# Kernel tuning notes

Measured on AMD Instinct MI355X. Metric: run time of the kernel, lower is better.

The kernel has to match this reference:

```python
import jax, jax.numpy as jnp
import numpy as np

N, E, F_IN, H, C = 50000, 800000, 128, 64, 10

def setup_inputs() -> dict:
    key = jax.random.key(0)
    ks = jax.random.split(key, 8)
    x = jax.random.normal(ks[0], (N, F_IN), dtype=jnp.float32)
    edge_index = jax.random.randint(ks[1], (2, E), 0, N, dtype=jnp.int32)
    edge_weight = jax.random.uniform(ks[2], (E,), dtype=jnp.float32)
    W1 = jax.random.normal(ks[3], (H, F_IN), dtype=jnp.float32) * 0.05
    W2 = jax.random.normal(ks[4], (H, H), dtype=jnp.float32) * 0.05
    W3 = jax.random.normal(ks[5], (C, H), dtype=jnp.float32) * 0.05
    b1 = jnp.zeros((H,), jnp.float32)
    b2 = jnp.zeros((H,), jnp.float32)
    b3 = jnp.zeros((C,), jnp.float32)
    return {"x": x, "edge_index": edge_index, "edge_weight": edge_weight,
            "W1": W1, "b1": b1, "W2": W2, "b2": b2, "W3": W3, "b3": b3}

def reference(x, edge_index, edge_weight, W1, b1, W2, b2, W3, b3):
    n = x.shape[0]
    row, col = edge_index[0], edge_index[1]
    # GCN symmetric normalization (add_self_loops=False): deg from edge weights on col
    deg = jax.ops.segment_sum(edge_weight, col, num_segments=n)  # [N]
    dinv = jnp.where(deg > 0, jax.lax.rsqrt(deg), 0.0)
    norm = dinv[row] * edge_weight * dinv[col]  # [E]

    def gcn_layer(h, W, b):
        h = h @ W.T                               # linear transform [N, out]
        msg = h[row] * norm[:, None]              # gather + scale   [E, out]
        agg = jax.ops.segment_sum(msg, col, num_segments=n)  # scatter-add [N, out]
        return agg + b

    h = gcn_layer(x, W1, b1)
    h = gcn_layer(h, W2, b2)
    logits = gcn_layer(h, W3, b3)
    soft = jax.nn.softmax(logits, axis=1)
    return logits, soft
```

## Files before the change

kernel.cpp:

```cpp
#include <hip/hip_runtime.h>
#include <hip/hip_fp16.h>

#define N_NODES 50000
#define N_EDGES 800000
#define F_IN    128
#define H_DIM   64
#define C_DIM   10
#define CPAD    16
#define CAP     48
#define BLOCK   256
#define BIN_NODES 256
#define NBINS   196
#define STRIDE  4480
#define E_BLK   2048
#define ABLOCKS ((N_EDGES + E_BLK - 1) / E_BLK)
#define DGB     (N_NODES / 16)
#define WB      ((N_NODES * 64) / 256)
#define POISON  ((int)0xAAAAAAAA)

__device__ __forceinline__ int unbase(int v) {
    return ((unsigned)v < 65536u) ? v : v - POISON;
}

__device__ __forceinline__ int   prow(unsigned v) { return (int)(v >> 16); }
__device__ __forceinline__ float pw(unsigned v)   {
    return __half2float(__ushort_as_half((unsigned short)(v & 0xFFFFu)));
}

__global__ __launch_bounds__(256) void k_binA(const int* __restrict__ rows,
                                              const int* __restrict__ cols,
                                              const float* __restrict__ ew,
                                              const float* __restrict__ W1,
                                              const float* __restrict__ b1,
                                              const float* __restrict__ W2,
                                              const float* __restrict__ b2,
                                              const float* __restrict__ W3,
                                              int* __restrict__ bucketCnt,
                                              unsigned* __restrict__ regionA,
                                              unsigned short* __restrict__ regionC,
                                              float* __restrict__ T2g,
                                              float* __restrict__ v1g,
                                              float* __restrict__ v2g) {
    const int tid = threadIdx.x;
    if (blockIdx.x < ABLOCKS) {
        __shared__ unsigned       sA[E_BLK];
        __shared__ unsigned short sC[E_BLK];
        __shared__ int hcnt[NBINS];
        __shared__ int lbase[NBINS];
        __shared__ int gb[NBINS];
        for (int i = tid; i < NBINS; i += BLOCK) hcnt[i] = 0;
        __syncthreads();

        const int e0 = blockIdx.x * E_BLK;
        unsigned rw[8];
        unsigned cl[8];
#pragma unroll
        for (int j = 0; j < 8; ++j) {
            int e = e0 + j * BLOCK + tid;
            if (e < N_EDGES) {
                int   c = cols[e];
                int   r = rows[e];
                float w = ew[e];
                rw[j] = ((unsigned)r << 16) | (unsigned)__half_as_ushort(__float2half(w));
                int lr = atomicAdd(&hcnt[c >> 8], 1);
                cl[j] = (unsigned)c | ((unsigned)lr << 16);
            } else {
                cl[j] = 0xFFFFFFFFu;
            }
        }
        __syncthreads();

        if (tid < 64) {
            int run = 0;
            for (int base = 0; base < NBINS; base += 64) {
                int i = base + tid;
                int v = (i < NBINS) ? hcnt[i] : 0;
                int s = v;
#pragma unroll
                for (int off = 1; off < 64; off <<= 1) {
                    int t = __shfl_up(s, off);
                    if (tid >= off) s += t;
                }
                if (i < NBINS) lbase[i] = run + s - v;
                run += __shfl(s, 63);
            }
        }
        __syncthreads();

#pragma unroll
        for (int j = 0; j < 8; ++j) {
            if (cl[j] != 0xFFFFFFFFu) {
                int c  = (int)(cl[j] & 0xFFFFu);
                int lr = (int)(cl[j] >> 16);
                int pos = lbase[c >> 8] + lr;
                sA[pos] = rw[j];
                sC[pos] = (unsigned short)c;
            }
        }
        if (tid < NBINS) gb[tid] = unbase(atomicAdd(&bucketCnt[tid], hcnt[tid]));
        __syncthreads();

        const int total = lbase[NBINS - 1] + hcnt[NBINS - 1];
        for (int i = tid; i < total; i += BLOCK) {
            int c = sC[i];
            int b = c >> 8;
            int gpos = gb[b] + (i - lbase[b]);
            if (gpos < STRIDE) {
                size_t p = (size_t)b * STRIDE + gpos;
                regionA[p] = sA[i];
                regionC[p] = (unsigned short)c;
            }
        }
        return;
    }

    __shared__ float u[C_DIM * H_DIM];
    for (int idx = tid; idx < C_DIM * H_DIM; idx += BLOCK) {
        int c = idx >> 6, j = idx & 63;
        float a = 0.f;
#pragma unroll
        for (int k = 0; k < H_DIM; ++k) a += W3[c * H_DIM + k] * W2[k * H_DIM + j];
        u[idx] = a;
    }
    __syncthreads();
    for (int idx = tid; idx < C_DIM * F_IN; idx += BLOCK) {
        int c = idx >> 7, f = idx & 127;
        float a = 0.f;
#pragma unroll
        for (int k = 0; k < H_DIM; ++k) a += u[c * H_DIM + k] * W1[k * F_IN + f];
        T2g[idx] = a;
    }
    if (tid < C_DIM) {
        float a = 0.f, b = 0.f;
#pragma unroll
        for (int k = 0; k < H_DIM; ++k) {
            a += u[tid * H_DIM + k] * b1[k];
            b += W3[tid * H_DIM + k] * b2[k];
        }
        v1g[tid] = a;
        v2g[tid] = b;
    }
}

__global__ __launch_bounds__(256) void k_binB(const int* __restrict__ bucketCnt,
                                              const unsigned* __restrict__ regionA,
                                              const unsigned short* __restrict__ regionC,
                                              float2* __restrict__ meta,
                                              unsigned* __restrict__ edata) {
    __shared__ unsigned sdata[BIN_NODES * CAP];
    __shared__ int   lcnt[BIN_NODES];
    __shared__ float wsum[BIN_NODES];
    const int tid = threadIdx.x;
    const int b   = blockIdx.x;
    if (tid < BIN_NODES) { lcnt[tid] = 0; wsum[tid] = 0.f; }
    __syncthreads();

    int tot = unbase(bucketCnt[b]);
    if (tot > STRIDE) tot = STRIDE;
    const size_t segBase = (size_t)b * STRIDE;
    for (int i = tid; i < tot; i += BLOCK) {
        unsigned e = regionA[segBase + i];
        int nl = (int)regionC[segBase + i] - b * BIN_NODES;
        int r = atomicAdd(&lcnt[nl], 1);
        if (r < CAP) sdata[nl * CAP + r] = e;
        atomicAdd(&wsum[nl], pw(e));
    }
    __syncthreads();

    const int n0 = b * BIN_NODES;
    const int nvalid = min(N_NODES - n0, BIN_NODES);
    if (tid < nvalid) {
        int c0 = min(lcnt[tid], CAP);
        int cp = (c0 + 15) & ~15;
        if (cp > CAP) cp = CAP;
        for (int r = c0; r < cp; ++r) sdata[tid * CAP + r] = 0u;
        float d = wsum[tid];
        meta[n0 + tid] = make_float2(d > 0.f ? rsqrtf(d) : 0.f, (float)cp);
    }
    __syncthreads();

    int4* dst = reinterpret_cast<int4*>(edata + (size_t)n0 * CAP);
    const int4* src = reinterpret_cast<const int4*>(sdata);
    const int nvec = nvalid * CAP / 4;
    for (int i = tid; i < nvec; i += BLOCK) dst[i] = src[i];
}

__global__ __launch_bounds__(256) void k_dg(const float* __restrict__ x,
                                            const float* __restrict__ T2g,
                                            const float2* __restrict__ meta,
                                            __half* __restrict__ bufA) {
    __shared__ float ts[16 * 132];
    __shared__ float xs[16][132];
    const int tid = threadIdx.x;
    const int n0 = blockIdx.x * 16;

    for (int i = tid; i < 16 * F_IN; i += BLOCK) {
        int c = i >> 7;
        ts[c * 132 + (i & 127)] = (c < C_DIM) ? T2g[i] : 0.f;
    }
    for (int i = tid; i < 16 * 32; i += BLOCK) {
        int ln = i >> 5, f4 = i & 31;
        float4 v = reinterpret_cast<const float4*>(x)[(n0 + ln) * 32 + f4];
        *reinterpret_cast<float4*>(&xs[ln][f4 * 4]) = v;
    }
    __syncthreads();

    const int g = tid >> 4;
    const int c = tid & 15;
    const int n = n0 + g;
    const float di = meta[n].x;

    const float4* tsv = reinterpret_cast<const float4*>(&ts[c * 132]);
    const float4* xv  = reinterpret_cast<const float4*>(&xs[g][0]);
    float a = 0.f;
#pragma unroll 8
    for (int f4 = 0; f4 < 32; ++f4) {
        float4 xx = xv[f4], tt = tsv[f4];
        a += xx.x * tt.x + xx.y * tt.y + xx.z * tt.z + xx.w * tt.w;
    }
    float outv = (c < C_DIM) ? a * di : (c == 10 ? di : 0.f);
    bufA[n * CPAD + c] = __float2half(outv);
}

__global__ __launch_bounds__(256) void k_gather(const float2* __restrict__ meta,
                                                const unsigned* __restrict__ edata,
                                                const __half* __restrict__ zin,
                                                __half* __restrict__ zout) {
    int n = (blockIdx.x * 256 + threadIdx.x) >> 6;
    if (n >= N_NODES) return;
    int lane = threadIdx.x & 63;
    int sub = lane >> 4, c = lane & 15;
    float2 m = meta[n];
    float di = m.x;
    int iters = ((int)m.y) >> 4;
    int base = n * CAP + sub;
    float acc = 0.f;
#pragma unroll
    for (int i = 0; i < 3; ++i) {
        if (i < iters) {
            int k = base + i * 16;
            unsigned e0 = edata[k];
            unsigned e1 = edata[k + 4];
            unsigned e2 = edata[k + 8];
            unsigned e3 = edata[k + 12];
            acc += pw(e0) * __half2float(zin[prow(e0) * CPAD + c]);
            acc += pw(e1) * __half2float(zin[prow(e1) * CPAD + c]);
            acc += pw(e2) * __half2float(zin[prow(e2) * CPAD + c]);
            acc += pw(e3) * __half2float(zin[prow(e3) * CPAD + c]);
        }
    }
    acc += __shfl_xor(acc, 32);
    acc += __shfl_xor(acc, 16);
    if (lane < 16) zout[n * CPAD + lane] = __float2half(acc * di * di);
}

__global__ __launch_bounds__(256) void k_final(const float2* __restrict__ meta,
                                               const unsigned* __restrict__ edata,
                                               const __half* __restrict__ zin,
                                               const __half* __restrict__ s1buf,
                                               const float* __restrict__ v1,
                                               const float* __restrict__ v2,
                                               const float* __restrict__ b3,
                                               float* __restrict__ logits,
                                               float* __restrict__ soft) {
    int n = (blockIdx.x * 256 + threadIdx.x) >> 6;
    if (n >= N_NODES) return;
    int lane = threadIdx.x & 63;
    int sub = lane >> 4, c = lane & 15;
    float2 m = meta[n];
    float di = m.x;
    int iters = ((int)m.y) >> 4;
    int base = n * CAP + sub;
    float acc = 0.f;
#pragma unroll
    for (int i = 0; i < 3; ++i) {
        if (i < iters) {
            int k = base + i * 16;
            unsigned e0 = edata[k];
            unsigned e1 = edata[k + 4];
            unsigned e2 = edata[k + 8];
            unsigned e3 = edata[k + 12];
            acc += pw(e0) * __half2float(zin[prow(e0) * CPAD + c]);
            acc += pw(e1) * __half2float(zin[prow(e1) * CPAD + c]);
            acc += pw(e2) * __half2float(zin[prow(e2) * CPAD + c]);
            acc += pw(e3) * __half2float(zin[prow(e3) * CPAD + c]);
        }
    }
    acc += __shfl_xor(acc, 32);
    acc += __shfl_xor(acc, 16);

    float r  = di > 0.f ? 1.0f / di : 0.f;
    float a1 = __half2float(s1buf[n * CPAD + 10]) * r;
    float a2 = __half2float(zin[n * CPAD + 10]) * r;
    float l = (c < C_DIM) ? di * acc + a2 * v1[c] + a1 * v2[c] + b3[c] : -1e30f;
    float mx = l;
#pragma unroll
    for (int d = 8; d >= 1; d >>= 1) mx = fmaxf(mx, __shfl_xor(mx, d));
    float ev = (c < C_DIM) ? __expf(l - mx) : 0.f;
    float s = ev;
#pragma unroll
    for (int d = 8; d >= 1; d >>= 1) s += __shfl_xor(s, d);
    if (lane < C_DIM) {
        logits[n * C_DIM + lane] = l;
        soft[n * C_DIM + lane]   = ev / s;
    }
}

extern "C" void kernel_launch(void* const* d_in, const int* in_sizes, int n_in,
                              void* d_out, int out_size, void* d_ws, size_t ws_size,
                              hipStream_t stream) {
    const float* x  = (const float*)d_in[0];
    const int*   ei = (const int*)d_in[1];
    const float* ew = (const float*)d_in[2];
    const float* W1 = (const float*)d_in[3];
    const float* b1 = (const float*)d_in[4];
    const float* W2 = (const float*)d_in[5];
    const float* b2 = (const float*)d_in[6];
    const float* W3 = (const float*)d_in[7];
    const float* b3 = (const float*)d_in[8];
    const int* rows = ei;
    const int* cols = ei + N_EDGES;

    char* ws = (char*)d_ws;
    size_t off = 0;
    auto alloc = [&](size_t bytes) { void* q = ws + off; off += (bytes + 15) & ~size_t(15); return q; };

    float2*         meta      = (float2*)         alloc((size_t)N_NODES * 8);
    __half*         bufA      = (__half*)         alloc((size_t)N_NODES * CPAD * 2);
    __half*         bufB      = (__half*)         alloc((size_t)N_NODES * CPAD * 2);
    float*          T2g       = (float*)          alloc(C_DIM * F_IN * 4);
    float*          v1        = (float*)          alloc(64);
    float*          v2        = (float*)          alloc(64);
    int*            bucketCnt = (int*)            alloc(NBINS * 4);
    unsigned*       regionA   = (unsigned*)       alloc((size_t)NBINS * STRIDE * 4);
    unsigned short* regionC   = (unsigned short*) alloc((size_t)NBINS * STRIDE * 2);
    unsigned*       edata     = (unsigned*)       alloc((size_t)N_NODES * CAP * 4);

    float* logits = (float*)d_out;
    float* soft   = logits + N_NODES * C_DIM;

    k_binA<<<ABLOCKS + 1, 256, 0, stream>>>(rows, cols, ew, W1, b1, W2, b2, W3,
                                            bucketCnt, regionA, regionC, T2g, v1, v2);
    k_binB<<<NBINS, 256, 0, stream>>>(bucketCnt, regionA, regionC, meta, edata);
    k_dg<<<DGB, 256, 0, stream>>>(x, T2g, meta, bufA);
    k_gather<<<WB, 256, 0, stream>>>(meta, edata, bufA, bufB);
    k_gather<<<WB, 256, 0, stream>>>(meta, edata, bufB, bufA);
    k_final<<<WB, 256, 0, stream>>>(meta, edata, bufA, bufB, v1, v2, b3,
                                    logits, soft);
}
```

Baseline: 166.7 us.

## Fuse projection, gather passes and softmax into one cooperative persistent kernel

Replaces the four separate launches (k_dg, two k_gather, k_final) with a single cooperative kernel that runs each stage in grid-stride loops and separates the stages with grid.sync(). This removes three kernel launch boundaries and their tail effects. It also halves the bin size used for edge bucketing (128 nodes per bin, more bins, smaller stride), which changes the binning stage's parallelism and shared-memory footprint. In exchange, grid-wide barriers cost something, and a persistent grid sized from occupancy may underuse the GPU compared with oversubscribed launches.

```diff
diff --git a/kernel.cpp b/kernel.cpp
--- a/kernel.cpp
+++ b/kernel.cpp
@@ -1,5 +1,8 @@
 #include <hip/hip_runtime.h>
 #include <hip/hip_fp16.h>
+#include <hip/hip_cooperative_groups.h>
+
+namespace cg = cooperative_groups;
 
 #define N_NODES 50000
 #define N_EDGES 800000
@@ -9,13 +12,12 @@
 #define CPAD    16
 #define CAP     48
 #define BLOCK   256
-#define BIN_NODES 256
-#define NBINS   196
-#define STRIDE  4480
+#define BIN_NODES 128
+#define NBINS   ((N_NODES + BIN_NODES - 1) / BIN_NODES)
+#define STRIDE  2560
 #define E_BLK   2048
 #define ABLOCKS ((N_EDGES + E_BLK - 1) / E_BLK)
 #define DGB     (N_NODES / 16)
-#define WB      ((N_NODES * 64) / 256)
 #define POISON  ((int)0xAAAAAAAA)
 
 __device__ __forceinline__ int unbase(int v) {
@@ -62,7 +64,7 @@
                 int   r = rows[e];
                 float w = ew[e];
                 rw[j] = ((unsigned)r << 16) | (unsigned)__half_as_ushort(__float2half(w));
-                int lr = atomicAdd(&hcnt[c >> 8], 1);
+                int lr = atomicAdd(&hcnt[c >> 7], 1);
                 cl[j] = (unsigned)c | ((unsigned)lr << 16);
             } else {
                 cl[j] = 0xFFFFFFFFu;
@@ -92,18 +94,19 @@
             if (cl[j] != 0xFFFFFFFFu) {
                 int c  = (int)(cl[j] & 0xFFFFu);
                 int lr = (int)(cl[j] >> 16);
-                int pos = lbase[c >> 8] + lr;
+                int pos = lbase[c >> 7] + lr;
                 sA[pos] = rw[j];
                 sC[pos] = (unsigned short)c;
             }
         }
-        if (tid < NBINS) gb[tid] = unbase(atomicAdd(&bucketCnt[tid], hcnt[tid]));
+        for (int i = tid; i < NBINS; i += BLOCK)
+            gb[i] = unbase(atomicAdd(&bucketCnt[i], hcnt[i]));
         __syncthreads();
 
         const int total = lbase[NBINS - 1] + hcnt[NBINS - 1];
         for (int i = tid; i < total; i += BLOCK) {
             int c = sC[i];
-            int b = c >> 8;
+            int b = c >> 7;
             int gpos = gb[b] + (i - lbase[b]);
             if (gpos < STRIDE) {
                 size_t p = (size_t)b * STRIDE + gpos;
@@ -185,124 +188,132 @@
     for (int i = tid; i < nvec; i += BLOCK) dst[i] = src[i];
 }
 
-__global__ __launch_bounds__(256) void k_dg(const float* __restrict__ x,
-                                            const float* __restrict__ T2g,
+__device__ __forceinline__ void gather_pass(int wid, int nW, int lane,
                                             const float2* __restrict__ meta,
-                                            __half* __restrict__ bufA) {
+                                            const unsigned* __restrict__ edata,
+                                            const __half* __restrict__ zin,
+                                            __half* __restrict__ zout) {
+    const int sub = lane >> 4, c = lane & 15;
+    for (int n = wid; n < N_NODES; n += nW) {
+        float2 m = meta[n];
+        int iters = ((int)m.y) >> 4;
+        int base = n * CAP + sub;
+        float acc = 0.f;
+#pragma unroll
+        for (int i = 0; i < 3; ++i) {
+            if (i < iters) {
+                int k = base + i * 16;
+                unsigned e0 = edata[k];
+                unsigned e1 = edata[k + 4];
+                unsigned e2 = edata[k + 8];
+                unsigned e3 = edata[k + 12];
+                acc += pw(e0) * __half2float(zin[prow(e0) * CPAD + c]);
+                acc += pw(e1) * __half2float(zin[prow(e1) * CPAD + c]);
+                acc += pw(e2) * __half2float(zin[prow(e2) * CPAD + c]);
+                acc += pw(e3) * __half2float(zin[prow(e3) * CPAD + c]);
+            }
+        }
+        acc += __shfl_xor(acc, 32);
+        acc += __shfl_xor(acc, 16);
+        if (lane < 16) zout[n * CPAD + lane] = __float2half(acc * m.x * m.x);
+    }
+}
+
+__global__ __launch_bounds__(256) void k_main(const float* __restrict__ x,
+                                              const float* __restrict__ T2g,
+                                              const float2* __restrict__ meta,
+                                              const unsigned* __restrict__ edata,
+                                              __half* __restrict__ bufA,
+                                              __half* __restrict__ bufB,
+                                              const float* __restrict__ v1,
+                                              const float* __restrict__ v2,
+                                              const float* __restrict__ b3,
+                                              float* __restrict__ logits,
+                                              float* __restrict__ soft) {
+    cg::grid_group grid = cg::this_grid();
+    const int tid  = threadIdx.x;
+    const int lane = tid & 63;
+    const int wid  = blockIdx.x * 4 + (tid >> 6);
+    const int nW   = gridDim.x * 4;
+
     __shared__ float ts[16 * 132];
     __shared__ float xs[16][132];
-    const int tid = threadIdx.x;
-    const int n0 = blockIdx.x * 16;
-
     for (int i = tid; i < 16 * F_IN; i += BLOCK) {
         int c = i >> 7;
         ts[c * 132 + (i & 127)] = (c < C_DIM) ? T2g[i] : 0.f;
     }
-    for (int i = tid; i < 16 * 32; i += BLOCK) {
-        int ln = i >> 5, f4 = i & 31;
-        float4 v = reinterpret_cast<const float4*>(x)[(n0 + ln) * 32 + f4];
-        *reinterpret_cast<float4*>(&xs[ln][f4 * 4]) = v;
-    }
-    __syncthreads();
-
-    const int g = tid >> 4;
-    const int c = tid & 15;
-    const int n = n0 + g;
-    const float di = meta[n].x;
-
-    const float4* tsv = reinterpret_cast<const float4*>(&ts[c * 132]);
-    const float4* xv  = reinterpret_cast<const float4*>(&xs[g][0]);
-    float a = 0.f;
+    const int g = tid >> 4, c = tid & 15;
+    for (int t = blockIdx.x; t < DGB; t += gridDim.x) {
+        __syncthreads();
+        const int n0 = t * 16;
+        for (int i = tid; i < 16 * 32; i += BLOCK) {
+            int ln = i >> 5, f4 = i & 31;
+            float4 v = reinterpret_cast<const float4*>(x)[(n0 + ln) * 32 + f4];
+            *reinterpret_cast<float4*>(&xs[ln][f4 * 4]) = v;
+        }
+        __syncthreads();
+        const int n = n0 + g;
+        const float di = meta[n].x;
+        const float4* tsv = reinterpret_cast<const float4*>(&ts[c * 132]);
+        const float4* xv  = reinterpret_cast<const float4*>(&xs[g][0]);
+        float a = 0.f;
 #pragma unroll 8
-    for (int f4 = 0; f4 < 32; ++f4) {
-        float4 xx = xv[f4], tt = tsv[f4];
-        a += xx.x * tt.x + xx.y * tt.y + xx.z * tt.z + xx.w * tt.w;
-    }
-    float outv = (c < C_DIM) ? a * di : (c == 10 ? di : 0.f);
-    bufA[n * CPAD + c] = __float2half(outv);
-}
-
-__global__ __launch_bounds__(256) void k_gather(const float2* __restrict__ meta,
-                                                const unsigned* __restrict__ edata,
-                                                const __half* __restrict__ zin,
-                                                __half* __restrict__ zout) {
-    int n = (blockIdx.x * 256 + threadIdx.x) >> 6;
-    if (n >= N_NODES) return;
-    int lane = threadIdx.x & 63;
-    int sub = lane >> 4, c = lane & 15;
-    float2 m = meta[n];
-    float di = m.x;
-    int iters = ((int)m.y) >> 4;
-    int base = n * CAP + sub;
-    float acc = 0.f;
-#pragma unroll
-    for (int i = 0; i < 3; ++i) {
-        if (i < iters) {
-            int k = base + i * 16;
-            unsigned e0 = edata[k];
-            unsigned e1 = edata[k + 4];
-            unsigned e2 = edata[k + 8];
-            unsigned e3 = edata[k + 12];
-            acc += pw(e0) * __half2float(zin[prow(e0) * CPAD + c]);
-            acc += pw(e1) * __half2float(zin[prow(e1) * CPAD + c]);
-            acc += pw(e2) * __half2float(zin[prow(e2) * CPAD + c]);
-            acc += pw(e3) * __half2float(zin[prow(e3) * CPAD + c]);
-        }
-    }
-    acc += __shfl_xor(acc, 32);
-    acc += __shfl_xor(acc, 16);
-    if (lane < 16) zout[n * CPAD + lane] = __float2half(acc * di * di);
-}
-
-__global__ __launch_bounds__(256) void k_final(const float2* __restrict__ meta,
-                                               const unsigned* __restrict__ edata,
-                                               const __half* __restrict__ zin,
-                                               const __half* __restrict__ s1buf,
-                                               const float* __restrict__ v1,
-                                               const float* __restrict__ v2,
-                                               const float* __restrict__ b3,
-                                               float* __restrict__ logits,
-                                               float* __restrict__ soft) {
-    int n = (blockIdx.x * 256 + threadIdx.x) >> 6;
-    if (n >= N_NODES) return;
-    int lane = threadIdx.x & 63;
-    int sub = lane >> 4, c = lane & 15;
-    float2 m = meta[n];
-    float di = m.x;
-    int iters = ((int)m.y) >> 4;
-    int base = n * CAP + sub;
-    float acc = 0.f;
-#pragma unroll
-    for (int i = 0; i < 3; ++i) {
-        if (i < iters) {
-            int k = base + i * 16;
-            unsigned e0 = edata[k];
-            unsigned e1 = edata[k + 4];
-            unsigned e2 = edata[k + 8];
-            unsigned e3 = edata[k + 12];
-            acc += pw(e0) * __half2float(zin[prow(e0) * CPAD + c]);
-            acc += pw(e1) * __half2float(zin[prow(e1) * CPAD + c]);
-            acc += pw(e2) * __half2float(zin[prow(e2) * CPAD + c]);
-            acc += pw(e3) * __half2float(zin[prow(e3) * CPAD + c]);
-        }
-    }
-    acc += __shfl_xor(acc, 32);
-    acc += __shfl_xor(acc, 16);
-
-    float r  = di > 0.f ? 1.0f / di : 0.f;
-    float a1 = __half2float(s1buf[n * CPAD + 10]) * r;
-    float a2 = __half2float(zin[n * CPAD + 10]) * r;
-    float l = (c < C_DIM) ? di * acc + a2 * v1[c] + a1 * v2[c] + b3[c] : -1e30f;
-    float mx = l;
-#pragma unroll
-    for (int d = 8; d >= 1; d >>= 1) mx = fmaxf(mx, __shfl_xor(mx, d));
-    float ev = (c < C_DIM) ? __expf(l - mx) : 0.f;
-    float s = ev;
-#pragma unroll
-    for (int d = 8; d >= 1; d >>= 1) s += __shfl_xor(s, d);
-    if (lane < C_DIM) {
-        logits[n * C_DIM + lane] = l;
-        soft[n * C_DIM + lane]   = ev / s;
+        for (int f4 = 0; f4 < 32; ++f4) {
+            float4 xx = xv[f4], tt = tsv[f4];
+            a += xx.x * tt.x + xx.y * tt.y + xx.z * tt.z + xx.w * tt.w;
+        }
+        float outv = (c < C_DIM) ? a * di : (c == 10 ? di : 0.f);
+        bufA[n * CPAD + c] = __float2half(outv);
+    }
+    grid.sync();
+
+    gather_pass(wid, nW, lane, meta, edata, bufA, bufB);
+    grid.sync();
+
+    gather_pass(wid, nW, lane, meta, edata, bufB, bufA);
+    grid.sync();
+
+    {
+        const int sub = lane >> 4, cc = lane & 15;
+        for (int n = wid; n < N_NODES; n += nW) {
+            float2 m = meta[n];
+            float di = m.x;
+            int iters = ((int)m.y) >> 4;
+            int base = n * CAP + sub;
+            float acc = 0.f;
+#pragma unroll
+            for (int i = 0; i < 3; ++i) {
+                if (i < iters) {
+                    int k = base + i * 16;
+                    unsigned e0 = edata[k];
+                    unsigned e1 = edata[k + 4];
+                    unsigned e2 = edata[k + 8];
+                    unsigned e3 = edata[k + 12];
+                    acc += pw(e0) * __half2float(bufA[prow(e0) * CPAD + cc]);
+                    acc += pw(e1) * __half2float(bufA[prow(e1) * CPAD + cc]);
+                    acc += pw(e2) * __half2float(bufA[prow(e2) * CPAD + cc]);
+                    acc += pw(e3) * __half2float(bufA[prow(e3) * CPAD + cc]);
+                }
+            }
+            acc += __shfl_xor(acc, 32);
+            acc += __shfl_xor(acc, 16);
+
+            float r  = di > 0.f ? 1.0f / di : 0.f;
+            float a1 = __half2float(bufB[n * CPAD + 10]) * r;
+            float a2 = __half2float(bufA[n * CPAD + 10]) * r;
+            float l = (cc < C_DIM) ? di * acc + a2 * v1[cc] + a1 * v2[cc] + b3[cc] : -1e30f;
+            float mx = l;
+#pragma unroll
+            for (int d = 8; d >= 1; d >>= 1) mx = fmaxf(mx, __shfl_xor(mx, d));
+            float ev = (cc < C_DIM) ? __expf(l - mx) : 0.f;
+            float s = ev;
+#pragma unroll
+            for (int d = 8; d >= 1; d >>= 1) s += __shfl_xor(s, d);
+            if (lane < C_DIM) {
+                logits[n * C_DIM + lane] = l;
+                soft[n * C_DIM + lane]   = ev / s;
+            }
+        }
     }
 }
 
@@ -339,12 +350,21 @@
     float* logits = (float*)d_out;
     float* soft   = logits + N_NODES * C_DIM;
 
-    k_binA<<<ABLOCKS + 1, 256, 0, stream>>>(rows, cols, ew, W1, b1, W2, b2, W3,
-                                            bucketCnt, regionA, regionC, T2g, v1, v2);
-    k_binB<<<NBINS, 256, 0, stream>>>(bucketCnt, regionA, regionC, meta, edata);
-    k_dg<<<DGB, 256, 0, stream>>>(x, T2g, meta, bufA);
-    k_gather<<<WB, 256, 0, stream>>>(meta, edata, bufA, bufB);
-    k_gather<<<WB, 256, 0, stream>>>(meta, edata, bufB, bufA);
-    k_final<<<WB, 256, 0, stream>>>(meta, edata, bufA, bufB, v1, v2, b3,
-                                    logits, soft);
-}
+    static int s_grid = 0;
+    if (s_grid == 0) {
+        int maxB = 0;
+        if (hipOccupancyMaxActiveBlocksPerMultiprocessor(&maxB, k_main, BLOCK, 0) != hipSuccess || maxB < 1)
+            maxB = 1;
+        s_grid = maxB * 256;
+        if (s_grid > 2048) s_grid = 2048;
+    }
+
+    k_binA<<<ABLOCKS + 1, BLOCK, 0, stream>>>(rows, cols, ew, W1, b1, W2, b2, W3,
+                                              bucketCnt, regionA, regionC, T2g, v1, v2);
+    k_binB<<<NBINS, BLOCK, 0, stream>>>(bucketCnt, regionA, regionC, meta, edata);
+
+    void* args[] = {(void*)&x, (void*)&T2g, (void*)&meta, (void*)&edata,
+                    (void*)&bufA, (void*)&bufB, (void*)&v1, (void*)&v2,
+                    (void*)&b3, (void*)&logits, (void*)&soft};
+    hipLaunchCooperativeKernel((void*)k_main, dim3(s_grid), dim3(BLOCK), args, 0, stream);
+}
```

Measured after the change: 553.1 us. 3.32x slower.

## Fuse first-layer dense projection into bin-B kernel and skip empty-bucket atomics

Applied to the files above, without the earlier changes.

Removes the separate k_dg launch. Each bin-B block now computes the x·T2 projection for its own 256 nodes, reading the degree inverse from shared memory instead of re-reading meta from global. It also skips the atomicAdd on bucket counters for bins with zero local count. The saved launch and the meta round-trip come at a cost: only 196 blocks now do the projection work serially over 16 tiles, which lowers parallelism for that phase, and bin-B needs more shared memory.

```diff
diff --git a/kernel.cpp b/kernel.cpp
--- a/kernel.cpp
+++ b/kernel.cpp
@@ -14,7 +14,6 @@
 #define STRIDE  4480
 #define E_BLK   2048
 #define ABLOCKS ((N_EDGES + E_BLK - 1) / E_BLK)
-#define DGB     (N_NODES / 16)
 #define WB      ((N_NODES * 64) / 256)
 #define POISON  ((int)0xAAAAAAAA)
 
@@ -97,7 +96,8 @@
                 sC[pos] = (unsigned short)c;
             }
         }
-        if (tid < NBINS) gb[tid] = unbase(atomicAdd(&bucketCnt[tid], hcnt[tid]));
+        if (tid < NBINS && hcnt[tid] > 0)
+            gb[tid] = unbase(atomicAdd(&bucketCnt[tid], hcnt[tid]));
         __syncthreads();
 
         const int total = lbase[NBINS - 1] + hcnt[NBINS - 1];
@@ -145,14 +145,24 @@
 __global__ __launch_bounds__(256) void k_binB(const int* __restrict__ bucketCnt,
                                               const unsigned* __restrict__ regionA,
                                               const unsigned short* __restrict__ regionC,
+                                              const float* __restrict__ x,
+                                              const float* __restrict__ T2g,
                                               float2* __restrict__ meta,
-                                              unsigned* __restrict__ edata) {
+                                              unsigned* __restrict__ edata,
+                                              __half* __restrict__ bufA) {
     __shared__ unsigned sdata[BIN_NODES * CAP];
     __shared__ int   lcnt[BIN_NODES];
     __shared__ float wsum[BIN_NODES];
+    __shared__ float dinvs[BIN_NODES];
+    __shared__ float ts[16 * 132];
+    __shared__ float xs[16][132];
     const int tid = threadIdx.x;
     const int b   = blockIdx.x;
     if (tid < BIN_NODES) { lcnt[tid] = 0; wsum[tid] = 0.f; }
+    for (int i = tid; i < 16 * F_IN; i += BLOCK) {
+        int c = i >> 7;
+        ts[c * 132 + (i & 127)] = (c < C_DIM) ? T2g[i] : 0.f;
+    }
     __syncthreads();
 
     int tot = unbase(bucketCnt[b]);
@@ -175,51 +185,46 @@
         if (cp > CAP) cp = CAP;
         for (int r = c0; r < cp; ++r) sdata[tid * CAP + r] = 0u;
         float d = wsum[tid];
-        meta[n0 + tid] = make_float2(d > 0.f ? rsqrtf(d) : 0.f, (float)cp);
+        float di = d > 0.f ? rsqrtf(d) : 0.f;
+        dinvs[tid] = di;
+        meta[n0 + tid] = make_float2(di, (float)cp);
     }
     __syncthreads();
 
-    int4* dst = reinterpret_cast<int4*>(edata + (size_t)n0 * CAP);
-    const int4* src = reinterpret_cast<const int4*>(sdata);
-    const int nvec = nvalid * CAP / 4;
-    for (int i = tid; i < nvec; i += BLOCK) dst[i] = src[i];
-}
-
-__global__ __launch_bounds__(256) void k_dg(const float* __restrict__ x,
-                                            const float* __restrict__ T2g,
-                                            const float2* __restrict__ meta,
-                                            __half* __restrict__ bufA) {
-    __shared__ float ts[16 * 132];
-    __shared__ float xs[16][132];
-    const int tid = threadIdx.x;
-    const int n0 = blockIdx.x * 16;
-
-    for (int i = tid; i < 16 * F_IN; i += BLOCK) {
-        int c = i >> 7;
-        ts[c * 132 + (i & 127)] = (c < C_DIM) ? T2g[i] : 0.f;
-    }
-    for (int i = tid; i < 16 * 32; i += BLOCK) {
-        int ln = i >> 5, f4 = i & 31;
-        float4 v = reinterpret_cast<const float4*>(x)[(n0 + ln) * 32 + f4];
-        *reinterpret_cast<float4*>(&xs[ln][f4 * 4]) = v;
-    }
-    __syncthreads();
-
-    const int g = tid >> 4;
-    const int c = tid & 15;
-    const int n = n0 + g;
-    const float di = meta[n].x;
-
-    const float4* tsv = reinterpret_cast<const float4*>(&ts[c * 132]);
-    const float4* xv  = reinterpret_cast<const float4*>(&xs[g][0]);
-    float a = 0.f;
+    {
+        int4* dst = reinterpret_cast<int4*>(edata + (size_t)n0 * CAP);
+        const int4* src = reinterpret_cast<const int4*>(sdata);
+        const int nvec = nvalid * CAP / 4;
+        for (int i = tid; i < nvec; i += BLOCK) dst[i] = src[i];
+    }
+
+    const int g = tid >> 4, c = tid & 15;
+    for (int t = 0; t < BIN_NODES / 16; ++t) {
+        __syncthreads();
+        const int n0t = n0 + t * 16;
+        for (int i = tid; i < 16 * 32; i += BLOCK) {
+            int ln = i >> 5, f4 = i & 31;
+            if (n0t + ln < N_NODES) {
+                float4 v = reinterpret_cast<const float4*>(x)[(n0t + ln) * 32 + f4];
+                *reinterpret_cast<float4*>(&xs[ln][f4 * 4]) = v;
+            }
+        }
+        __syncthreads();
+        const int n = n0t + g;
+        if (n < N_NODES) {
+            const float di = dinvs[t * 16 + g];
+            const float4* tsv = reinterpret_cast<const float4*>(&ts[c * 132]);
+            const float4* xv  = reinterpret_cast<const float4*>(&xs[g][0]);
+            float a = 0.f;
 #pragma unroll 8
-    for (int f4 = 0; f4 < 32; ++f4) {
-        float4 xx = xv[f4], tt = tsv[f4];
-        a += xx.x * tt.x + xx.y * tt.y + xx.z * tt.z + xx.w * tt.w;
-    }
-    float outv = (c < C_DIM) ? a * di : (c == 10 ? di : 0.f);
-    bufA[n * CPAD + c] = __float2half(outv);
+            for (int f4 = 0; f4 < 32; ++f4) {
+                float4 xx = xv[f4], tt = tsv[f4];
+                a += xx.x * tt.x + xx.y * tt.y + xx.z * tt.z + xx.w * tt.w;
+            }
+            float outv = (c < C_DIM) ? a * di : (c == 10 ? di : 0.f);
+            bufA[n * CPAD + c] = __float2half(outv);
+        }
+    }
 }
 
 __global__ __launch_bounds__(256) void k_gather(const float2* __restrict__ meta,
@@ -339,12 +344,12 @@
     float* logits = (float*)d_out;
     float* soft   = logits + N_NODES * C_DIM;
 
-    k_binA<<<ABLOCKS + 1, 256, 0, stream>>>(rows, cols, ew, W1, b1, W2, b2, W3,
-                                            bucketCnt, regionA, regionC, T2g, v1, v2);
-    k_binB<<<NBINS, 256, 0, stream>>>(bucketCnt, regionA, regionC, meta, edata);
-    k_dg<<<DGB, 256, 0, stream>>>(x, T2g, meta, bufA);
-    k_gather<<<WB, 256, 0, stream>>>(meta, edata, bufA, bufB);
-    k_gather<<<WB, 256, 0, stream>>>(meta, edata, bufB, bufA);
-    k_final<<<WB, 256, 0, stream>>>(meta, edata, bufA, bufB, v1, v2, b3,
-                                    logits, soft);
-}
+    k_binA<<<ABLOCKS + 1, BLOCK, 0, stream>>>(rows, cols, ew, W1, b1, W2, b2, W3,
+                                              bucketCnt, regionA, regionC, T2g, v1, v2);
+    k_binB<<<NBINS, BLOCK, 0, stream>>>(bucketCnt, regionA, regionC, x, T2g,
+                                        meta, edata, bufA);
+    k_gather<<<WB, BLOCK, 0, stream>>>(meta, edata, bufA, bufB);
+    k_gather<<<WB, BLOCK, 0, stream>>>(meta, edata, bufB, bufA);
+    k_final<<<WB, BLOCK, 0, stream>>>(meta, edata, bufA, bufB, v1, v2, b3,
+                                      logits, soft);
+}
```

Result: slower. 178.8 us (+7.2%).

## Shrink node bins to 64 and use fixed-trip vectorized edge gathers

Applied to the files above, without the earlier changes.

Edge binning now uses 64-node bins, giving about 782 buckets instead of 196. This spreads the per-bin CSR build in k_binB over far more workgroups. The gather and final kernels drop the per-node trip count and always process all 48 zero-padded slots with uint4 loads. The per-node metadata shrinks to a single dinv float. In exchange, every node pays for three gather iterations even when its degree is low, and the wider shared-memory histogram in k_binA adds more scan and atomic work.

```diff
diff --git a/kernel.cpp b/kernel.cpp
--- a/kernel.cpp
+++ b/kernel.cpp
@@ -9,9 +9,9 @@
 #define CPAD    16
 #define CAP     48
 #define BLOCK   256
-#define BIN_NODES 256
-#define NBINS   196
-#define STRIDE  4480
+#define BIN_NODES 64
+#define NBINS   ((N_NODES + BIN_NODES - 1) / BIN_NODES)
+#define STRIDE  1280
 #define E_BLK   2048
 #define ABLOCKS ((N_EDGES + E_BLK - 1) / E_BLK)
 #define DGB     (N_NODES / 16)
@@ -62,7 +62,7 @@
                 int   r = rows[e];
                 float w = ew[e];
                 rw[j] = ((unsigned)r << 16) | (unsigned)__half_as_ushort(__float2half(w));
-                int lr = atomicAdd(&hcnt[c >> 8], 1);
+                int lr = atomicAdd(&hcnt[c >> 6], 1);
                 cl[j] = (unsigned)c | ((unsigned)lr << 16);
             } else {
                 cl[j] = 0xFFFFFFFFu;
@@ -92,18 +92,19 @@
             if (cl[j] != 0xFFFFFFFFu) {
                 int c  = (int)(cl[j] & 0xFFFFu);
                 int lr = (int)(cl[j] >> 16);
-                int pos = lbase[c >> 8] + lr;
+                int pos = lbase[c >> 6] + lr;
                 sA[pos] = rw[j];
                 sC[pos] = (unsigned short)c;
             }
         }
-        if (tid < NBINS) gb[tid] = unbase(atomicAdd(&bucketCnt[tid], hcnt[tid]));
+        for (int i = tid; i < NBINS; i += BLOCK)
+            if (hcnt[i] > 0) gb[i] = unbase(atomicAdd(&bucketCnt[i], hcnt[i]));
         __syncthreads();
 
         const int total = lbase[NBINS - 1] + hcnt[NBINS - 1];
         for (int i = tid; i < total; i += BLOCK) {
             int c = sC[i];
-            int b = c >> 8;
+            int b = c >> 6;
             int gpos = gb[b] + (i - lbase[b]);
             if (gpos < STRIDE) {
                 size_t p = (size_t)b * STRIDE + gpos;
@@ -145,7 +146,7 @@
 __global__ __launch_bounds__(256) void k_binB(const int* __restrict__ bucketCnt,
                                               const unsigned* __restrict__ regionA,
                                               const unsigned short* __restrict__ regionC,
-                                              float2* __restrict__ meta,
+                                              float* __restrict__ dinv,
                                               unsigned* __restrict__ edata) {
     __shared__ unsigned sdata[BIN_NODES * CAP];
     __shared__ int   lcnt[BIN_NODES];
@@ -171,23 +172,21 @@
     const int nvalid = min(N_NODES - n0, BIN_NODES);
     if (tid < nvalid) {
         int c0 = min(lcnt[tid], CAP);
-        int cp = (c0 + 15) & ~15;
-        if (cp > CAP) cp = CAP;
-        for (int r = c0; r < cp; ++r) sdata[tid * CAP + r] = 0u;
+        for (int r = c0; r < CAP; ++r) sdata[tid * CAP + r] = 0u;
         float d = wsum[tid];
-        meta[n0 + tid] = make_float2(d > 0.f ? rsqrtf(d) : 0.f, (float)cp);
+        dinv[n0 + tid] = d > 0.f ? rsqrtf(d) : 0.f;
     }
     __syncthreads();
 
     int4* dst = reinterpret_cast<int4*>(edata + (size_t)n0 * CAP);
     const int4* src = reinterpret_cast<const int4*>(sdata);
-    const int nvec = nvalid * CAP / 4;
+    const int nvec = nvalid * (CAP / 4);
     for (int i = tid; i < nvec; i += BLOCK) dst[i] = src[i];
 }
 
 __global__ __launch_bounds__(256) void k_dg(const float* __restrict__ x,
                                             const float* __restrict__ T2g,
-                                            const float2* __restrict__ meta,
+                                            const float* __restrict__ dinv,
                                             __half* __restrict__ bufA) {
     __shared__ float ts[16 * 132];
     __shared__ float xs[16][132];
@@ -208,7 +207,7 @@
     const int g = tid >> 4;
     const int c = tid & 15;
     const int n = n0 + g;
-    const float di = meta[n].x;
+    const float di = dinv[n];
 
     const float4* tsv = reinterpret_cast<const float4*>(&ts[c * 132]);
     const float4* xv  = reinterpret_cast<const float4*>(&xs[g][0]);
@@ -222,7 +221,7 @@
     bufA[n * CPAD + c] = __float2half(outv);
 }
 
-__global__ __launch_bounds__(256) void k_gather(const float2* __restrict__ meta,
+__global__ __launch_bounds__(256) void k_gather(const float* __restrict__ dinv,
                                                 const unsigned* __restrict__ edata,
                                                 const __half* __restrict__ zin,
                                                 __half* __restrict__ zout) {
@@ -230,31 +229,23 @@
     if (n >= N_NODES) return;
     int lane = threadIdx.x & 63;
     int sub = lane >> 4, c = lane & 15;
-    float2 m = meta[n];
-    float di = m.x;
-    int iters = ((int)m.y) >> 4;
-    int base = n * CAP + sub;
+    const uint4* bp = reinterpret_cast<const uint4*>(edata + n * CAP) + sub;
     float acc = 0.f;
 #pragma unroll
     for (int i = 0; i < 3; ++i) {
-        if (i < iters) {
-            int k = base + i * 16;
-            unsigned e0 = edata[k];
-            unsigned e1 = edata[k + 4];
-            unsigned e2 = edata[k + 8];
-            unsigned e3 = edata[k + 12];
-            acc += pw(e0) * __half2float(zin[prow(e0) * CPAD + c]);
-            acc += pw(e1) * __half2float(zin[prow(e1) * CPAD + c]);
-            acc += pw(e2) * __half2float(zin[prow(e2) * CPAD + c]);
-            acc += pw(e3) * __half2float(zin[prow(e3) * CPAD + c]);
-        }
+        uint4 e = bp[i * 4];
+        acc += pw(e.x) * __half2float(zin[prow(e.x) * CPAD + c]);
+        acc += pw(e.y) * __half2float(zin[prow(e.y) * CPAD + c]);
+        acc += pw(e.z) * __half2float(zin[prow(e.z) * CPAD + c]);
+        acc += pw(e.w) * __half2float(zin[prow(e.w) * CPAD + c]);
     }
     acc += __shfl_xor(acc, 32);
     acc += __shfl_xor(acc, 16);
+    float di = dinv[n];
     if (lane < 16) zout[n * CPAD + lane] = __float2half(acc * di * di);
 }
 
-__global__ __launch_bounds__(256) void k_final(const float2* __restrict__ meta,
+__global__ __launch_bounds__(256) void k_final(const float* __restrict__ dinv,
                                                const unsigned* __restrict__ edata,
                                                const __half* __restrict__ zin,
                                                const __half* __restrict__ s1buf,
@@ -267,28 +258,20 @@
     if (n >= N_NODES) return;
     int lane = threadIdx.x & 63;
     int sub = lane >> 4, c = lane & 15;
-    float2 m = meta[n];
-    float di = m.x;
-    int iters = ((int)m.y) >> 4;
-    int base = n * CAP + sub;
+    const uint4* bp = reinterpret_cast<const uint4*>(edata + n * CAP) + sub;
     float acc = 0.f;
 #pragma unroll
     for (int i = 0; i < 3; ++i) {
-        if (i < iters) {
-            int k = base + i * 16;
-            unsigned e0 = edata[k];
-            unsigned e1 = edata[k + 4];
-            unsigned e2 = edata[k + 8];
-            unsigned e3 = edata[k + 12];
-            acc += pw(e0) * __half2float(zin[prow(e0) * CPAD + c]);
-            acc += pw(e1) * __half2float(zin[prow(e1) * CPAD + c]);
-            acc += pw(e2) * __half2float(zin[prow(e2) * CPAD + c]);
-            acc += pw(e3) * __half2float(zin[prow(e3) * CPAD + c]);
-        }
+        uint4 e = bp[i * 4];
+        acc += pw(e.x) * __half2float(zin[prow(e.x) * CPAD + c]);
+        acc += pw(e.y) * __half2float(zin[prow(e.y) * CPAD + c]);
+        acc += pw(e.z) * __half2float(zin[prow(e.z) * CPAD + c]);
+        acc += pw(e.w) * __half2float(zin[prow(e.w) * CPAD + c]);
     }
     acc += __shfl_xor(acc, 32);
     acc += __shfl_xor(acc, 16);
 
+    float di = dinv[n];
     float r  = di > 0.f ? 1.0f / di : 0.f;
     float a1 = __half2float(s1buf[n * CPAD + 10]) * r;
     float a2 = __half2float(zin[n * CPAD + 10]) * r;
@@ -325,7 +308,7 @@
     size_t off = 0;
     auto alloc = [&](size_t bytes) { void* q = ws + off; off += (bytes + 15) & ~size_t(15); return q; };
 
-    float2*         meta      = (float2*)         alloc((size_t)N_NODES * 8);
+    float*          dinv      = (float*)          alloc((size_t)N_NODES * 4);
     __half*         bufA      = (__half*)         alloc((size_t)N_NODES * CPAD * 2);
     __half*         bufB      = (__half*)         alloc((size_t)N_NODES * CPAD * 2);
     float*          T2g       = (float*)          alloc(C_DIM * F_IN * 4);
@@ -339,12 +322,12 @@
     float* logits = (float*)d_out;
     float* soft   = logits + N_NODES * C_DIM;
 
-    k_binA<<<ABLOCKS + 1, 256, 0, stream>>>(rows, cols, ew, W1, b1, W2, b2, W3,
-                                            bucketCnt, regionA, regionC, T2g, v1, v2);
-    k_binB<<<NBINS, 256, 0, stream>>>(bucketCnt, regionA, regionC, meta, edata);
-    k_dg<<<DGB, 256, 0, stream>>>(x, T2g, meta, bufA);
-    k_gather<<<WB, 256, 0, stream>>>(meta, edata, bufA, bufB);
-    k_gather<<<WB, 256, 0, stream>>>(meta, edata, bufB, bufA);
-    k_final<<<WB, 256, 0, stream>>>(meta, edata, bufA, bufB, v1, v2, b3,
-                                    logits, soft);
-}
+    k_binA<<<ABLOCKS + 1, BLOCK, 0, stream>>>(rows, cols, ew, W1, b1, W2, b2, W3,
+                                              bucketCnt, regionA, regionC, T2g, v1, v2);
+    k_binB<<<NBINS, BLOCK, 0, stream>>>(bucketCnt, regionA, regionC, dinv, edata);
+    k_dg<<<DGB, BLOCK, 0, stream>>>(x, T2g, dinv, bufA);
+    k_gather<<<WB, BLOCK, 0, stream>>>(dinv, edata, bufA, bufB);
+    k_gather<<<WB, BLOCK, 0, stream>>>(dinv, edata, bufB, bufA);
+    k_final<<<WB, BLOCK, 0, stream>>>(dinv, edata, bufA, bufB, v1, v2, b3,
+                                      logits, soft);
+}
```

New measurement: 169.0 us. Within noise of the previous version (+1.4%).
